# Kernel optimization log

Measured on AMD Instinct MI355X. Metric: run time of the kernel, lower is better.

The kernel has to match this reference:

```python
import jax, jax.numpy as jnp
import numpy as np

V, L, H, D, T, B = 32000, 8, 16, 1024, 1024, 2
HD = D // H
SCALE = 1.0 / float(np.sqrt(HD))


def setup_inputs() -> dict:
    key = jax.random.key(0)
    ks = jax.random.split(key, 8)
    s = 0.02
    def n(k, shape):
        return jax.random.normal(k, shape, jnp.float32) * s
    return {
        "input_ids": jax.random.randint(ks[0], (B, T), 0, V),
        "tok_emb": n(ks[1], (V, D)),            # tied with lm_head
        "pos_emb": n(ks[2], (T, D)),
        "ln1_w": jnp.ones((L, D)), "ln1_b": jnp.zeros((L, D)),
        "qkv_w": n(ks[3], (L, D, 3 * D)),       # no bias in qkv_proj
        "out_w": n(ks[4], (L, D, D)), "out_b": jnp.zeros((L, D)),
        "ln2_w": jnp.ones((L, D)), "ln2_b": jnp.zeros((L, D)),
        "fc1_w": n(ks[5], (L, D, 4 * D)), "fc1_b": jnp.zeros((L, 4 * D)),
        "fc2_w": n(ks[6], (L, 4 * D, D)), "fc2_b": jnp.zeros((L, D)),
        "lnf_w": jnp.ones((D,)), "lnf_b": jnp.zeros((D,)),
    }


def _ln(x, w, b):
    m = x.mean(-1, keepdims=True)
    v = x.var(-1, keepdims=True)
    return (x - m) * jax.lax.rsqrt(v + 1e-5) * w + b


def _gpt(input_ids, tok_emb, pos_emb, ln1_w, ln1_b, qkv_w, out_w, out_b,
         ln2_w, ln2_b, fc1_w, fc1_b, fc2_w, fc2_b, lnf_w, lnf_b):
    Bq, Tq = input_ids.shape
    x = tok_emb[input_ids] + pos_emb[:Tq][None]          # [B,T,D]
    causal = jnp.tril(jnp.ones((Tq, Tq), bool))          # [T,T]

    def layer(x, p):
        l1w, l1b, qw, ow, ob, l2w, l2b, f1w, f1b, f2w, f2b = p
        h = _ln(x, l1w, l1b)
        qkv = h @ qw                                     # [B,T,3D]
        q, k, v = jnp.split(qkv, 3, axis=-1)
        q = q.reshape(Bq, Tq, H, HD)
        k = k.reshape(Bq, Tq, H, HD)
        v = v.reshape(Bq, Tq, H, HD)
        att = jnp.einsum('bqhd,bkhd->bhqk', q, k) * SCALE
        att = jnp.where(causal, att, -jnp.inf)
        att = jax.nn.softmax(att, axis=-1)
        o = jnp.einsum('bhqk,bkhd->bqhd', att, v).reshape(Bq, Tq, D)
        x = x + o @ ow + ob
        h2 = _ln(x, l2w, l2b)
        x = x + jax.nn.gelu(h2 @ f1w + f1b, approximate=False) @ f2w + f2b
        return x, None

    x, _ = jax.lax.scan(layer, x, (ln1_w, ln1_b, qkv_w, out_w, out_b,
                                   ln2_w, ln2_b, fc1_w, fc1_b, fc2_w, fc2_b))
    x = _ln(x, lnf_w, lnf_b)
    return x @ tok_emb.T                                 # tied lm_head


def reference(input_ids, tok_emb, pos_emb, ln1_w, ln1_b, qkv_w, out_w, out_b,
              ln2_w, ln2_b, fc1_w, fc1_b, fc2_w, fc2_b, lnf_w, lnf_b):
    return _gpt(input_ids, tok_emb, pos_emb, ln1_w, ln1_b, qkv_w, out_w, out_b,
                ln2_w, ln2_b, fc1_w, fc1_b, fc2_w, fc2_b, lnf_w, lnf_b)
```

## Files before the change

### kernel.cpp

```cpp
#include <hip/hip_runtime.h>
#include <hip/hip_bf16.h>
#include <math.h>


#define DEV_INLINE __device__ __forceinline__

typedef float  f32x4  __attribute__((ext_vector_type(4)));
typedef __bf16 bf16x8 __attribute__((ext_vector_type(8)));
typedef short  s16x4  __attribute__((ext_vector_type(4)));
typedef short  s16x8  __attribute__((ext_vector_type(8)));
typedef unsigned int u32x4 __attribute__((ext_vector_type(4)));

#define BBATCH 2
#define TSEQ   1024
#define DMODEL 1024
#define NHEAD  16
#define HDIM   64
#define NLAYER 8
#define NVOCAB 32000
#define MTOK   (BBATCH*TSEQ)

DEV_INLINE short f2bf(float f) {
    __bf16 h = (__bf16)f;
    union { __bf16 h; short s; } u; u.h = h; return u.s;
}

typedef const __attribute__((address_space(1))) unsigned int* gas_t;
typedef __attribute__((address_space(3))) unsigned int* las_t;
DEV_INLINE void llds16(const void* g, void* l) {
    __builtin_amdgcn_global_load_lds((gas_t)g, (las_t)l, 16, 0, 0);
}

#define BAR()  asm volatile("s_barrier" ::: "memory")
#define VMW4() asm volatile("s_waitcnt vmcnt(4)" ::: "memory")
#define VMW2() asm volatile("s_waitcnt vmcnt(2)" ::: "memory")
#define VMW0() asm volatile("s_waitcnt vmcnt(0)" ::: "memory")

__global__ __launch_bounds__(256) void flash_k(
    const short* __restrict__ qkv, const short* __restrict__ Vt,
    short* __restrict__ O)
{
    const int qb = blockIdx.x;
    const int z  = blockIdx.y;
    const int zb = z >> 4, zh = z & 15;

    __shared__ short Qs[128 * 64];
    __shared__ short KP[128 * 136];
    __shared__ short Vs[64 * 128];

    const int tid  = threadIdx.x;
    const int w    = tid >> 6, lane = tid & 63;
    const int lr   = lane & 15, kg = lane >> 4;

    const long long qbase = (long long)zb * TSEQ * 3072;
    const short* Qg = qkv + qbase + zh * HDIM;
    const short* Kg = qkv + qbase + DMODEL + zh * HDIM;
    const short* Vg = Vt + (long long)z * (HDIM * TSEQ);

    const int sr   = tid >> 3, pc = tid & 7;
    const int lc   = pc ^ (sr & 7);
    const int sr16 = tid >> 4, pc16 = tid & 15;

    {
        const short* qp = Qg + (long long)(qb * 128 + sr) * 3072 + lc * 8;
        const short* kp = Kg + (long long)(0 + sr) * 3072 + lc * 8;
        #pragma unroll
        for (int it = 0; it < 4; ++it) {
            llds16(qp + (long long)it * 32 * 3072, Qs + tid * 8 + it * 2048);
            llds16(kp + (long long)it * 32 * 3072, KP + tid * 8 + it * 2048);
        }
        #pragma unroll
        for (int it = 0; it < 4; ++it) {
            const int r = it * 16 + sr16;
            const int lc2 = pc16 ^ (r & 7);
            llds16(Vg + (long long)r * TSEQ + 0 + lc2 * 8, Vs + tid * 8 + it * 2048);
        }
    }
    __syncthreads();
    bf16x8 afq[2][2];
    #pragma unroll
    for (int s = 0; s < 2; ++s)
        #pragma unroll
        for (int i = 0; i < 2; ++i) {
            const int r = w * 32 + i * 16 + lr;
            afq[s][i] = *(const bf16x8*)&Qs[r * 64 + (((s * 4 + kg) ^ (r & 7)) << 3)];
        }

    f32x4 aco[2][4] = {};
    float m_[2][4], l_[2][4];
    #pragma unroll
    for (int i = 0; i < 2; ++i)
        #pragma unroll
        for (int p = 0; p < 4; ++p) { m_[i][p] = -1e30f; l_[i][p] = 0.f; }

    const int nt = qb + 1;
    for (int t = 0; t < nt; ++t) {
        u32x4 kpre[4], vpre[4];
        const bool nx = (t + 1 < nt);
        if (nx) {
            const int kn = (t + 1) * 128;
            #pragma unroll
            for (int it = 0; it < 4; ++it)
                kpre[it] = *(const u32x4*)(Kg + (long long)(kn + sr + it * 32) * 3072 + lc * 8);
            #pragma unroll
            for (int it = 0; it < 4; ++it) {
                const int r = it * 16 + sr16;
                const int lc2 = pc16 ^ (r & 7);
                vpre[it] = *(const u32x4*)(Vg + (long long)r * TSEQ + kn + lc2 * 8);
            }
            __builtin_amdgcn_sched_barrier(0);
        }

        f32x4 acs[2][8] = {};
        #pragma unroll
        for (int s = 0; s < 2; ++s)
            #pragma unroll
            for (int j = 0; j < 8; ++j) {
                const int rk = j * 16 + lr;
                bf16x8 bk = *(const bf16x8*)&KP[rk * 64 + (((s * 4 + kg) ^ (rk & 7)) << 3)];
                #pragma unroll
                for (int i = 0; i < 2; ++i)
                    acs[i][j] = __builtin_amdgcn_mfma_f32_16x16x32_bf16(
                        afq[s][i], bk, acs[i][j], 0, 0, 0);
            }

        #pragma unroll
        for (int i = 0; i < 2; ++i)
            #pragma unroll
            for (int j = 0; j < 8; ++j)
                #pragma unroll
                for (int p = 0; p < 4; ++p) {
                    float v = acs[i][j][p] * 0.125f;
                    if (t == qb && (j * 16 + lr) > (w * 32 + i * 16 + kg * 4 + p))
                        v = -1e30f;
                    acs[i][j][p] = v;
                }

        float sc[2][4];
        #pragma unroll
        for (int i = 0; i < 2; ++i)
            #pragma unroll
            for (int p = 0; p < 4; ++p) {
                float r = acs[i][0][p];
                #pragma unroll
                for (int j = 1; j < 8; ++j) r = fmaxf(r, acs[i][j][p]);
                r = fmaxf(r, __shfl_xor(r, 1, 64));
                r = fmaxf(r, __shfl_xor(r, 2, 64));
                r = fmaxf(r, __shfl_xor(r, 4, 64));
                r = fmaxf(r, __shfl_xor(r, 8, 64));
                const float mn = fmaxf(m_[i][p], r);
                sc[i][p] = __expf(m_[i][p] - mn);
                m_[i][p] = mn;
            }
        #pragma unroll
        for (int i = 0; i < 2; ++i)
            #pragma unroll
            for (int j = 0; j < 8; ++j)
                #pragma unroll
                for (int p = 0; p < 4; ++p)
                    acs[i][j][p] = __expf(acs[i][j][p] - m_[i][p]);
        #pragma unroll
        for (int i = 0; i < 2; ++i)
            #pragma unroll
            for (int p = 0; p < 4; ++p) {
                float s = 0.f;
                #pragma unroll
                for (int j = 0; j < 8; ++j) s += acs[i][j][p];
                s += __shfl_xor(s, 1, 64);
                s += __shfl_xor(s, 2, 64);
                s += __shfl_xor(s, 4, 64);
                s += __shfl_xor(s, 8, 64);
                l_[i][p] = l_[i][p] * sc[i][p] + s;
            }
        #pragma unroll
        for (int i = 0; i < 2; ++i)
            #pragma unroll
            for (int j2 = 0; j2 < 4; ++j2)
                #pragma unroll
                for (int p = 0; p < 4; ++p)
                    aco[i][j2][p] *= sc[i][p];

        __syncthreads();

        #pragma unroll
        for (int i = 0; i < 2; ++i)
            #pragma unroll
            for (int j = 0; j < 8; ++j)
                #pragma unroll
                for (int p = 0; p < 4; ++p)
                    KP[(w * 32 + i * 16 + kg * 4 + p) * 136 + j * 16 + lr] =
                        f2bf(acs[i][j][p]);
        __syncthreads();

        #pragma unroll
        for (int ks = 0; ks < 4; ++ks) {
            bf16x8 pa[2], pb[4];
            #pragma unroll
            for (int i = 0; i < 2; ++i)
                pa[i] = *(const bf16x8*)&KP[(w * 32 + i * 16 + lr) * 136 + ks * 32 + kg * 8];
            #pragma unroll
            for (int j2 = 0; j2 < 4; ++j2) {
                const int d = j2 * 16 + lr;
                pb[j2] = *(const bf16x8*)&Vs[d * 128 + (((ks * 4 + kg) ^ (d & 7)) << 3)];
            }
            #pragma unroll
            for (int i = 0; i < 2; ++i)
                #pragma unroll
                for (int j2 = 0; j2 < 4; ++j2)
                    aco[i][j2] = __builtin_amdgcn_mfma_f32_16x16x32_bf16(
                        pa[i], pb[j2], aco[i][j2], 0, 0, 0);
        }
        __syncthreads();

        if (nx) {
            #pragma unroll
            for (int it = 0; it < 4; ++it)
                *(u32x4*)(KP + tid * 8 + it * 2048) = kpre[it];
            #pragma unroll
            for (int it = 0; it < 4; ++it)
                *(u32x4*)(Vs + tid * 8 + it * 2048) = vpre[it];
            __syncthreads();
        }
    }

    #pragma unroll
    for (int i = 0; i < 2; ++i)
        #pragma unroll
        for (int j2 = 0; j2 < 4; ++j2)
            #pragma unroll
            for (int p = 0; p < 4; ++p) {
                const int row = zb * TSEQ + qb * 128 + w * 32 + i * 16 + kg * 4 + p;
                const int col = zh * HDIM + j2 * 16 + lr;
                O[(long long)row * DMODEL + col] = f2bf(aco[i][j2][p] / l_[i][p]);
            }
}

__global__ __launch_bounds__(512, 2) void gemm256_k(
    const short* __restrict__ A, const short* __restrict__ B,
    float* __restrict__ C, int K, int lda, int ldb, int ldc, int gx)
{
    extern __shared__ short smem[];

    const int nwg = gridDim.x;
    int wg = blockIdx.x;
    int sw = (wg & 7) * (nwg >> 3) + (wg >> 3);
    const int bx = sw >> 3, by = sw & 7;
    const int bn0 = bx * 256, bm0 = by * 256;

    const int tid  = threadIdx.x;
    const int w    = tid >> 6, lane = tid & 63;
    const int wm   = w >> 2, wn = w & 3;
    const int lr   = lane & 15, kg = lane >> 4;

    const int r0  = tid >> 3;
    const int pc  = tid & 7;
    const int lc0 = pc ^ (r0 & 7);
    const int r1  = r0 + 64;
    const int lc1 = pc ^ (r1 & 7);

    f32x4 acc[2][2][4][2] = {};
    const int nk = K >> 6;

    auto stage = [&](int buf, int isA, int h, int kk) {
        const short* gp = isA ? A : B;
        const int    ld = isA ? lda : ldb;
        const long long rb = (long long)((isA ? bm0 : bn0) + h * 128);
        short* lp = smem + buf * 32768 + (isA ? 0 : 16384) + h * 8192;
        llds16(gp + (rb + r0) * ld + kk + lc0 * 8, lp + w * 512);
        llds16(gp + (rb + r1) * ld + kk + lc1 * 8, lp + 4096 + w * 512);
    };

#define PHASE(BUF, QM, QN, ISA, H, DOWAIT)                                      \
    do {                                                                        \
        const short* Ah = smem + (BUF) * 32768 + (QM) * 8192;                   \
        const short* Bh = smem + (BUF) * 32768 + 16384 + (QN) * 8192;           \
        bf16x8 af[2][4], bfr[2][2];                                             \
        _Pragma("unroll")                                                       \
        for (int s2 = 0; s2 < 2; ++s2) {                                        \
            _Pragma("unroll")                                                   \
            for (int i = 0; i < 4; ++i) {                                       \
                const int ra = wm * 64 + i * 16 + lr;                           \
                af[s2][i] = *(const bf16x8*)                                    \
                    &Ah[ra * 64 + (((s2 * 4 + kg) ^ (ra & 7)) << 3)];           \
            }                                                                   \
            _Pragma("unroll")                                                   \
            for (int j = 0; j < 2; ++j) {                                       \
                const int rb2 = wn * 32 + j * 16 + lr;                          \
                bfr[s2][j] = *(const bf16x8*)                                   \
                    &Bh[rb2 * 64 + (((s2 * 4 + kg) ^ (rb2 & 7)) << 3)];         \
            }                                                                   \
        }                                                                       \
        if (pf) stage(nb, ISA, H, kk);                                          \
        BAR();                                                                  \
        __builtin_amdgcn_s_setprio(1);                                          \
        _Pragma("unroll")                                                       \
        for (int s2 = 0; s2 < 2; ++s2)                                          \
            _Pragma("unroll")                                                   \
            for (int i = 0; i < 4; ++i)                                         \
                _Pragma("unroll")                                               \
                for (int j = 0; j < 2; ++j)                                     \
                    acc[QM][QN][i][j] = __builtin_amdgcn_mfma_f32_16x16x32_bf16(\
                        af[s2][i], bfr[s2][j], acc[QM][QN][i][j], 0, 0, 0);     \
        __builtin_amdgcn_s_setprio(0);                                          \
        DOWAIT;                                                                 \
        BAR();                                                                  \
    } while (0)

    stage(0, 1, 0, 0);
    stage(0, 0, 0, 0);
    stage(0, 1, 1, 0);
    stage(0, 0, 1, 0);
    if (nk > 1) { VMW4(); } else { VMW0(); }
    BAR();

    for (int t = 0; t < nk - 1; ++t) {
        const int  buf = t & 1, nb = buf ^ 1;
        const int  kk  = (t + 1) << 6;
        const bool pf  = true;
        PHASE(buf, 0, 0, 1, 0, VMW4());
        PHASE(buf, 1, 0, 0, 0, VMW4());
        PHASE(buf, 1, 1, 1, 1, (void)0);
        PHASE(buf, 0, 1, 0, 1, VMW4());
    }
    {
        const int  buf = (nk - 1) & 1, nb = buf ^ 1; (void)nb;
        const int  kk  = 0;
        const bool pf  = false;
        PHASE(buf, 0, 0, 1, 0, VMW2());
        PHASE(buf, 1, 0, 0, 0, VMW0());
        PHASE(buf, 1, 1, 1, 1, (void)0);
        PHASE(buf, 0, 1, 0, 1, (void)0);
    }
#undef PHASE

    #pragma unroll
    for (int qm = 0; qm < 2; ++qm)
        #pragma unroll
        for (int qn = 0; qn < 2; ++qn)
            #pragma unroll
            for (int i = 0; i < 4; ++i)
                #pragma unroll
                for (int j = 0; j < 2; ++j) {
                    const int gr = bm0 + qm * 128 + wm * 64 + i * 16 + kg * 4;
                    const int gc = bn0 + qn * 128 + wn * 32 + j * 16 + lr;
                    #pragma unroll
                    for (int p = 0; p < 4; ++p)
                        C[(long long)(gr + p) * ldc + gc] = acc[qm][qn][i][j][p];
                }
}

template<int BN, int EPI>
__global__ __launch_bounds__(256) void gemm_k(
    const short* __restrict__ Ag, const short* __restrict__ Bg,
    void* __restrict__ Cg, const float* __restrict__ bias,
    const float* __restrict__ resid,
    int M, int N, int K, int lda, int ldb, int ldc,
    long long sAz, long long sBz, long long sCz,
    float scale, int swz)
{
    int bx = blockIdx.x, by = blockIdx.y;
    if (swz) {
        const int gx = gridDim.x;
        const int nwg = gx * gridDim.y;
        if ((nwg & 7) == 0) {
            int wg = by * gx + bx;
            int wg2 = (wg & 7) * (nwg >> 3) + (wg >> 3);
            bx = wg2 % gx; by = wg2 / gx;
        }
    }
    const int bn0 = bx * BN, bm0 = by * 128;
    const int zz = blockIdx.z;

    const short* A = Ag + zz * sAz;
    const short* B = Bg + zz * sBz;

    __shared__ short Als[128 * 64];
    __shared__ short Bls[BN * 64];

    const int tid  = threadIdx.x;
    const int lane = tid & 63;
    const int wave = tid >> 6;
    constexpr int WMS = (BN == 128) ? 64 : 32;
    constexpr int MI  = (BN == 128) ? 4 : 2;
    constexpr int NJ  = 4;
    const int wm = (BN == 128) ? (wave >> 1) : wave;
    const int wn = (BN == 128) ? (wave & 1) : 0;
    const int lr = lane & 15, kg = lane >> 4;
    const int xv = (lr & 7) << 4;

    const int sr = tid >> 3;
    const int sc = (tid & 7) ^ (sr & 7);
    const short* aP = A + (long long)(bm0 + sr) * lda + sc * 8;
    const short* bP = B + (long long)(bn0 + sr) * ldb + sc * 8;
    short* aL = &Als[wave * 512];
    short* bL = &Bls[wave * 512];

    f32x4 acc[MI][NJ] = {};
    const int nk = K >> 6;

    for (int kt = 0; kt < nk; ++kt) {
        const int k0 = kt << 6;
        #pragma unroll
        for (int it = 0; it < 4; ++it)
            llds16(aP + (long long)it * 32 * lda + k0, aL + it * 2048);
        #pragma unroll
        for (int it = 0; it < BN / 32; ++it)
            llds16(bP + (long long)it * 32 * ldb + k0, bL + it * 2048);
        __syncthreads();

        #pragma unroll
        for (int s = 0; s < 2; ++s) {
            const int ofs = (((s << 6) | (kg << 4)) ^ xv) >> 1;
            bf16x8 af[MI], bf[NJ];
            #pragma unroll
            for (int i = 0; i < MI; ++i)
                af[i] = *(const bf16x8*)&Als[(wm * WMS + i * 16 + lr) * 64 + ofs];
            #pragma unroll
            for (int j = 0; j < NJ; ++j)
                bf[j] = *(const bf16x8*)&Bls[(wn * 64 + j * 16 + lr) * 64 + ofs];
            #pragma unroll
            for (int i = 0; i < MI; ++i)
                #pragma unroll
                for (int j = 0; j < NJ; ++j)
                    acc[i][j] = __builtin_amdgcn_mfma_f32_16x16x32_bf16(
                        af[i], bf[j], acc[i][j], 0, 0, 0);
        }
        __syncthreads();
    }

    short* Cs = (short*)Cg + zz * sCz;
    float* Cf = (float*)Cg + zz * sCz;
    #pragma unroll
    for (int i = 0; i < MI; ++i) {
        #pragma unroll
        for (int j = 0; j < NJ; ++j) {
            const int gr = bm0 + wm * WMS + i * 16 + kg * 4;
            const int gc = bn0 + wn * 64 + j * 16 + lr;
            #pragma unroll
            for (int p = 0; p < 4; ++p) {
                const long long off = (long long)(gr + p) * ldc + gc;
                float v = acc[i][j][p];
                if (EPI == 0) {
                    Cf[off] = v;
                } else if (EPI == 1) {
                    Cs[off] = f2bf(v * scale);
                } else if (EPI == 2) {
                    Cf[off] = v + bias[gc] + resid[off];
                } else {
                    v += bias[gc];
                    v = 0.5f * v * (1.0f + erff(v * 0.70710678118654752f));
                    Cs[off] = f2bf(v);
                }
            }
        }
    }
}

__global__ __launch_bounds__(256) void freduce_k(
    const float* __restrict__ p0, const float* __restrict__ p1,
    const float* __restrict__ bias, float* __restrict__ x)
{
    const long long idx = ((long long)blockIdx.x * 256 + threadIdx.x) * 4;
    const int col = (int)(idx & (DMODEL - 1));
    float4 a = *(const float4*)&p0[idx];
    float4 b = *(const float4*)&p1[idx];
    float4 c = *(const float4*)&x[idx];
    float4 bb = *(const float4*)&bias[col];
    float4 o;
    o.x = c.x + a.x + b.x + bb.x;
    o.y = c.y + a.y + b.y + bb.y;
    o.z = c.z + a.z + b.z + bb.z;
    o.w = c.w + a.w + b.w + bb.w;
    *(float4*)&x[idx] = o;
}

__global__ __launch_bounds__(256) void embed_k(
    const int* __restrict__ ids, const float* __restrict__ tok,
    const float* __restrict__ pos, float* __restrict__ x)
{
    const int gid = blockIdx.x * 256 + threadIdx.x;
    const int row = gid >> 8;
    const int c   = (gid & 255) << 2;
    const int t   = row & (TSEQ - 1);
    const int id  = ids[row];
    const float4 a = *(const float4*)&tok[(long long)id * DMODEL + c];
    const float4 p = *(const float4*)&pos[(long long)t * DMODEL + c];
    float4 o; o.x = a.x + p.x; o.y = a.y + p.y; o.z = a.z + p.z; o.w = a.w + p.w;
    *(float4*)&x[(long long)row * DMODEL + c] = o;
}

__global__ __launch_bounds__(256) void ln_k(
    const float* __restrict__ x, const float* __restrict__ w,
    const float* __restrict__ b, short* __restrict__ o)
{
    const int row  = blockIdx.x * 4 + (threadIdx.x >> 6);
    const int lane = threadIdx.x & 63;
    const float* xp = x + (long long)row * DMODEL + lane * 16;
    float4 v[4];
    #pragma unroll
    for (int q = 0; q < 4; ++q) v[q] = *(const float4*)(xp + q * 4);
    float s = 0.f, s2 = 0.f;
    #pragma unroll
    for (int q = 0; q < 4; ++q) {
        s  += v[q].x + v[q].y + v[q].z + v[q].w;
        s2 += v[q].x * v[q].x + v[q].y * v[q].y + v[q].z * v[q].z + v[q].w * v[q].w;
    }
    #pragma unroll
    for (int d = 1; d < 64; d <<= 1) {
        s  += __shfl_xor(s, d, 64);
        s2 += __shfl_xor(s2, d, 64);
    }
    const float mean = s * (1.0f / DMODEL);
    const float var  = s2 * (1.0f / DMODEL) - mean * mean;
    const float rs   = rsqrtf(var + 1e-5f);
    const float* wp = w + lane * 16;
    const float* bp = b + lane * 16;
    short ov[16];
    #pragma unroll
    for (int q = 0; q < 4; ++q) {
        float4 wv = *(const float4*)(wp + q * 4);
        float4 bv = *(const float4*)(bp + q * 4);
        ov[q * 4 + 0] = f2bf((v[q].x - mean) * rs * wv.x + bv.x);
        ov[q * 4 + 1] = f2bf((v[q].y - mean) * rs * wv.y + bv.y);
        ov[q * 4 + 2] = f2bf((v[q].z - mean) * rs * wv.z + bv.z);
        ov[q * 4 + 3] = f2bf((v[q].w - mean) * rs * wv.w + bv.w);
    }
    short* op = o + (long long)row * DMODEL + lane * 16;
    *(s16x8*)op       = *(s16x8*)&ov[0];
    *(s16x8*)(op + 8) = *(s16x8*)&ov[8];
}

template<typename T>
DEV_INLINE void tcvt_body(const T* sp, short* dp, int lds_, int ldd,
                          int bx, int by, short (*ls)[68], int t)
{
    const int tr0 = by * 64, tc0 = bx * 64;
    const int rr = t >> 4, cc = (t & 15) * 4;
    #pragma unroll
    for (int q = 0; q < 4; ++q) {
        const int r = q * 16 + rr;
        if constexpr (sizeof(T) == 4) {
            float4 v = *(const float4*)&sp[(long long)(tr0 + r) * lds_ + tc0 + cc];
            ls[cc + 0][r] = f2bf(v.x); ls[cc + 1][r] = f2bf(v.y);
            ls[cc + 2][r] = f2bf(v.z); ls[cc + 3][r] = f2bf(v.w);
        } else {
            s16x4 v = *(const s16x4*)&sp[(long long)(tr0 + r) * lds_ + tc0 + cc];
            ls[cc + 0][r] = v[0]; ls[cc + 1][r] = v[1];
            ls[cc + 2][r] = v[2]; ls[cc + 3][r] = v[3];
        }
    }
    __syncthreads();
    #pragma unroll
    for (int q = 0; q < 4; ++q) {
        const int c = q * 16 + rr;
        s16x4 v;
        v[0] = ls[c][cc]; v[1] = ls[c][cc + 1]; v[2] = ls[c][cc + 2]; v[3] = ls[c][cc + 3];
        *(s16x4*)&dp[(long long)(tc0 + c) * ldd + tr0 + cc] = v;
    }
}

template<typename T>
__global__ __launch_bounds__(256) void tcvt_k(
    const T* __restrict__ src, short* __restrict__ dst,
    int lds_, int ldd, int Hdiv,
    long long sSb, long long sSh, long long sDb, long long sDh)
{
    __shared__ short ls[64][68];
    const int z = blockIdx.z, zb = z / Hdiv, zh = z - zb * Hdiv;
    tcvt_body<T>(src + zb * sSb + zh * sSh, dst + zb * sDb + zh * sDh,
                 lds_, ldd, blockIdx.x, blockIdx.y, ls, threadIdx.x);
}

__global__ __launch_bounds__(256) void wcvt_k(
    const float* __restrict__ qw, const float* __restrict__ ow,
    const float* __restrict__ f1, const float* __restrict__ f2,
    short* __restrict__ wq, short* __restrict__ wo,
    short* __restrict__ w1, short* __restrict__ w2)
{
    __shared__ short ls[64][68];
    const int id = blockIdx.x;
    const float* src; short* dst; int lds_, ldd, bx, by;
    if (id < 768)       { src = qw; dst = wq; lds_ = 3072; ldd = 1024; bx = id % 48;  by = id / 48; }
    else if (id < 1024) { int i = id - 768;  src = ow; dst = wo; lds_ = 1024; ldd = 1024; bx = i % 16; by = i / 16; }
    else if (id < 2048) { int i = id - 1024; src = f1; dst = w1; lds_ = 4096; ldd = 1024; bx = i % 64; by = i / 64; }
    else                { int i = id - 2048; src = f2; dst = w2; lds_ = 1024; ldd = 4096; bx = i % 16; by = i / 16; }
    tcvt_body<float>(src, dst, lds_, ldd, bx, by, ls, threadIdx.x);
}

__global__ __launch_bounds__(256) void cvt_k(
    const float* __restrict__ s, short* __restrict__ d, int n4)
{
    int i = blockIdx.x * 256 + threadIdx.x;
    const int stride = gridDim.x * 256;
    for (; i < n4; i += stride) {
        float4 v = *(const float4*)&s[(long long)i * 4];
        s16x4 o = { f2bf(v.x), f2bf(v.y), f2bf(v.z), f2bf(v.w) };
        *(s16x4*)&d[(long long)i * 4] = o;
    }
}

extern "C" void kernel_launch(void* const* d_in, const int* in_sizes, int n_in,
                              void* d_out, int out_size, void* d_ws, size_t ws_size,
                              hipStream_t stream)
{
    const int*   ids  = (const int*)  d_in[0];
    const float* tok  = (const float*)d_in[1];
    const float* pos  = (const float*)d_in[2];
    const float* ln1w = (const float*)d_in[3];
    const float* ln1b = (const float*)d_in[4];
    const float* qkvw = (const float*)d_in[5];
    const float* outw = (const float*)d_in[6];
    const float* outb = (const float*)d_in[7];
    const float* ln2w = (const float*)d_in[8];
    const float* ln2b = (const float*)d_in[9];
    const float* fc1w = (const float*)d_in[10];
    const float* fc1b = (const float*)d_in[11];
    const float* fc2w = (const float*)d_in[12];
    const float* fc2b = (const float*)d_in[13];
    const float* lnfw = (const float*)d_in[14];
    const float* lnfb = (const float*)d_in[15];
    float* out = (float*)d_out;

    char* ws = (char*)d_ws;
    const size_t MB = 1024 * 1024;
    float* x    = (float*)(ws);
    short* hb   = (short*)(ws + 8  * MB);
    short* qkvb = (short*)(ws + 12 * MB);
    short* g    = (short*)(ws + 24 * MB);
    short* Vt   = (short*)(ws + 40 * MB);
    float* fp   = (float*)(ws + 44 * MB);
    short* tokb = (short*)(ws + 12 * MB);

    const bool big = ws_size >= (size_t)267 * MB;
    short* wq = (short*)(ws + 75 * MB);
    short *wo, *w1, *w2;
    if (big) {
        wo = (short*)(ws + 123 * MB);
        w1 = (short*)(ws + 139 * MB);
        w2 = (short*)(ws + 203 * MB);
    } else {
        wo = (short*)(ws + 81 * MB);
        w1 = (short*)(ws + 83 * MB);
        w2 = (short*)(ws + 91 * MB);
    }

    const long long LWQ = 3072LL * 1024, LWO = 1024LL * 1024;
    const long long LW1 = 4096LL * 1024, LW2 = 1024LL * 4096;

    hipFuncSetAttribute((const void*)gemm256_k,
                        hipFuncAttributeMaxDynamicSharedMemorySize, 131072);

    dim3 blk(256);
    embed_k<<<MTOK, blk, 0, stream>>>(ids, tok, pos, x);

    if (big) {
        tcvt_k<float><<<dim3(48, 16, 8), blk, 0, stream>>>(qkvw, wq, 3072, 1024, 1, LWQ, 0, LWQ, 0);
        tcvt_k<float><<<dim3(16, 16, 8), blk, 0, stream>>>(outw, wo, 1024, 1024, 1, LWO, 0, LWO, 0);
        tcvt_k<float><<<dim3(64, 16, 8), blk, 0, stream>>>(fc1w, w1, 4096, 1024, 1, LW1, 0, LW1, 0);
        tcvt_k<float><<<dim3(16, 64, 8), blk, 0, stream>>>(fc2w, w2, 1024, 4096, 1, LW2, 0, LW2, 0);
    }

    for (int l = 0; l < NLAYER; ++l) {
        short* wql = wq + (big ? l * LWQ : 0);
        short* wol = wo + (big ? l * LWO : 0);
        short* w1l = w1 + (big ? l * LW1 : 0);
        short* w2l = w2 + (big ? l * LW2 : 0);
        if (!big)
            wcvt_k<<<3072, blk, 0, stream>>>(
                qkvw + l * LWQ, outw + l * LWO, fc1w + l * LW1, fc2w + l * LW2,
                wql, wol, w1l, w2l);

        ln_k<<<MTOK / 4, blk, 0, stream>>>(x, ln1w + l * DMODEL, ln1b + l * DMODEL, hb);

        gemm_k<128, 1><<<dim3(24, 16, 1), blk, 0, stream>>>(
            hb, wql, qkvb, nullptr, nullptr,
            MTOK, 3 * DMODEL, DMODEL, DMODEL, DMODEL, 3 * DMODEL,
            0, 0, 0, 1.0f, 1);

        tcvt_k<short><<<dim3(1, 16, BBATCH * NHEAD), blk, 0, stream>>>(
            qkvb + 2 * DMODEL, Vt, 3 * DMODEL, TSEQ, NHEAD,
            (long long)TSEQ * 3 * DMODEL, HDIM,
            (long long)NHEAD * HDIM * TSEQ, (long long)HDIM * TSEQ);

        flash_k<<<dim3(8, BBATCH * NHEAD), blk, 0, stream>>>(qkvb, Vt, hb);

        gemm_k<64, 2><<<dim3(16, 16, 1), blk, 0, stream>>>(
            hb, wol, x, outb + l * DMODEL, x,
            MTOK, DMODEL, DMODEL, DMODEL, DMODEL, DMODEL,
            0, 0, 0, 1.0f, 1);

        ln_k<<<MTOK / 4, blk, 0, stream>>>(x, ln2w + l * DMODEL, ln2b + l * DMODEL, hb);

        gemm_k<128, 3><<<dim3(32, 16, 1), blk, 0, stream>>>(
            hb, w1l, g, fc1b + (long long)l * 4 * DMODEL, nullptr,
            MTOK, 4 * DMODEL, DMODEL, DMODEL, DMODEL, 4 * DMODEL,
            0, 0, 0, 1.0f, 1);

        gemm_k<128, 0><<<dim3(8, 16, 2), blk, 0, stream>>>(
            g, w2l, fp, nullptr, nullptr,
            MTOK, DMODEL, 2048, 4 * DMODEL, 4 * DMODEL, DMODEL,
            2048, 2048, (long long)MTOK * DMODEL, 1.0f, 1);
        freduce_k<<<MTOK, blk, 0, stream>>>(
            fp, fp + (long long)MTOK * DMODEL, fc2b + l * DMODEL, x);
    }

    ln_k<<<MTOK / 4, blk, 0, stream>>>(x, lnfw, lnfb, hb);

    cvt_k<<<2048, blk, 0, stream>>>(tok, tokb, NVOCAB * DMODEL / 4);

    gemm256_k<<<dim3((NVOCAB / 256) * (MTOK / 256)), dim3(512), 131072, stream>>>(
        hb, tokb, out, DMODEL, DMODEL, DMODEL, NVOCAB, NVOCAB / 256);
}
```

Before: 1.786 ms.

## Double-buffer GEMM LDS staging and fuse residual reduce with LayerNorm

The generic GEMM now double-buffers its LDS tiles, issuing the next K-tile's global-to-LDS loads before computing the current one and dropping one barrier per iteration. The out-projection switches to a split-K GEMM with two partial outputs. Those partials are combined in a new kernel that adds bias and residual and also applies the following LayerNorm, so the standalone LN kernels and the embed kernel are merged away. This cuts launches and extra passes over the activations, at the cost of doubled LDS use (which may lower occupancy) and an extra fp32 partial buffer write and read for the out-projection.

```diff
diff --git a/kernel.cpp b/kernel.cpp
--- a/kernel.cpp
+++ b/kernel.cpp
@@ -35,6 +35,17 @@
 #define VMW4() asm volatile("s_waitcnt vmcnt(4)" ::: "memory")
 #define VMW2() asm volatile("s_waitcnt vmcnt(2)" ::: "memory")
 #define VMW0() asm volatile("s_waitcnt vmcnt(0)" ::: "memory")
+
+DEV_INLINE float block_sum(float v) {
+    __shared__ float sb[4];
+    #pragma unroll
+    for (int o = 32; o > 0; o >>= 1) v += __shfl_down(v, o, 64);
+    if ((threadIdx.x & 63) == 0) sb[threadIdx.x >> 6] = v;
+    __syncthreads();
+    float r = sb[0] + sb[1] + sb[2] + sb[3];
+    __syncthreads();
+    return r;
+}
 
 __global__ __launch_bounds__(256) void flash_k(
     const short* __restrict__ qkv, const short* __restrict__ Vt,
@@ -353,7 +364,6 @@
 __global__ __launch_bounds__(256) void gemm_k(
     const short* __restrict__ Ag, const short* __restrict__ Bg,
     void* __restrict__ Cg, const float* __restrict__ bias,
-    const float* __restrict__ resid,
     int M, int N, int K, int lda, int ldb, int ldc,
     long long sAz, long long sBz, long long sCz,
     float scale, int swz)
@@ -374,8 +384,8 @@
     const short* A = Ag + zz * sAz;
     const short* B = Bg + zz * sBz;
 
-    __shared__ short Als[128 * 64];
-    __shared__ short Bls[BN * 64];
+    __shared__ short Als[2][128 * 64];
+    __shared__ short Bls[2][BN * 64];
 
     const int tid  = threadIdx.x;
     const int lane = tid & 63;
@@ -392,21 +402,28 @@
     const int sc = (tid & 7) ^ (sr & 7);
     const short* aP = A + (long long)(bm0 + sr) * lda + sc * 8;
     const short* bP = B + (long long)(bn0 + sr) * ldb + sc * 8;
-    short* aL = &Als[wave * 512];
-    short* bL = &Bls[wave * 512];
 
     f32x4 acc[MI][NJ] = {};
     const int nk = K >> 6;
 
-    for (int kt = 0; kt < nk; ++kt) {
+    auto stage = [&](int buf, int kt) {
         const int k0 = kt << 6;
+        short* aL = &Als[buf][wave * 512];
+        short* bL = &Bls[buf][wave * 512];
         #pragma unroll
         for (int it = 0; it < 4; ++it)
             llds16(aP + (long long)it * 32 * lda + k0, aL + it * 2048);
         #pragma unroll
         for (int it = 0; it < BN / 32; ++it)
             llds16(bP + (long long)it * 32 * ldb + k0, bL + it * 2048);
-        __syncthreads();
+    };
+
+    stage(0, 0);
+    __syncthreads();
+
+    for (int kt = 0; kt < nk; ++kt) {
+        const int cb = kt & 1;
+        if (kt + 1 < nk) stage(cb ^ 1, kt + 1);
 
         #pragma unroll
         for (int s = 0; s < 2; ++s) {
@@ -414,10 +431,10 @@
             bf16x8 af[MI], bf[NJ];
             #pragma unroll
             for (int i = 0; i < MI; ++i)
-                af[i] = *(const bf16x8*)&Als[(wm * WMS + i * 16 + lr) * 64 + ofs];
+                af[i] = *(const bf16x8*)&Als[cb][(wm * WMS + i * 16 + lr) * 64 + ofs];
             #pragma unroll
             for (int j = 0; j < NJ; ++j)
-                bf[j] = *(const bf16x8*)&Bls[(wn * 64 + j * 16 + lr) * 64 + ofs];
+                bf[j] = *(const bf16x8*)&Bls[cb][(wn * 64 + j * 16 + lr) * 64 + ofs];
             #pragma unroll
             for (int i = 0; i < MI; ++i)
                 #pragma unroll
@@ -444,8 +461,6 @@
                     Cf[off] = v;
                 } else if (EPI == 1) {
                     Cs[off] = f2bf(v * scale);
-                } else if (EPI == 2) {
-                    Cf[off] = v + bias[gc] + resid[off];
                 } else {
                     v += bias[gc];
                     v = 0.5f * v * (1.0f + erff(v * 0.70710678118654752f));
@@ -456,78 +471,73 @@
     }
 }
 
-__global__ __launch_bounds__(256) void freduce_k(
+__global__ __launch_bounds__(256) void fredln_k(
     const float* __restrict__ p0, const float* __restrict__ p1,
-    const float* __restrict__ bias, float* __restrict__ x)
-{
-    const long long idx = ((long long)blockIdx.x * 256 + threadIdx.x) * 4;
-    const int col = (int)(idx & (DMODEL - 1));
-    float4 a = *(const float4*)&p0[idx];
-    float4 b = *(const float4*)&p1[idx];
-    float4 c = *(const float4*)&x[idx];
-    float4 bb = *(const float4*)&bias[col];
-    float4 o;
-    o.x = c.x + a.x + b.x + bb.x;
-    o.y = c.y + a.y + b.y + bb.y;
-    o.z = c.z + a.z + b.z + bb.z;
-    o.w = c.w + a.w + b.w + bb.w;
-    *(float4*)&x[idx] = o;
-}
-
-__global__ __launch_bounds__(256) void embed_k(
-    const int* __restrict__ ids, const float* __restrict__ tok,
-    const float* __restrict__ pos, float* __restrict__ x)
-{
-    const int gid = blockIdx.x * 256 + threadIdx.x;
-    const int row = gid >> 8;
-    const int c   = (gid & 255) << 2;
-    const int t   = row & (TSEQ - 1);
-    const int id  = ids[row];
-    const float4 a = *(const float4*)&tok[(long long)id * DMODEL + c];
-    const float4 p = *(const float4*)&pos[(long long)t * DMODEL + c];
-    float4 o; o.x = a.x + p.x; o.y = a.y + p.y; o.z = a.z + p.z; o.w = a.w + p.w;
-    *(float4*)&x[(long long)row * DMODEL + c] = o;
-}
-
-__global__ __launch_bounds__(256) void ln_k(
-    const float* __restrict__ x, const float* __restrict__ w,
-    const float* __restrict__ b, short* __restrict__ o)
-{
-    const int row  = blockIdx.x * 4 + (threadIdx.x >> 6);
-    const int lane = threadIdx.x & 63;
-    const float* xp = x + (long long)row * DMODEL + lane * 16;
-    float4 v[4];
-    #pragma unroll
-    for (int q = 0; q < 4; ++q) v[q] = *(const float4*)(xp + q * 4);
-    float s = 0.f, s2 = 0.f;
-    #pragma unroll
-    for (int q = 0; q < 4; ++q) {
-        s  += v[q].x + v[q].y + v[q].z + v[q].w;
-        s2 += v[q].x * v[q].x + v[q].y * v[q].y + v[q].z * v[q].z + v[q].w * v[q].w;
-    }
-    #pragma unroll
-    for (int d = 1; d < 64; d <<= 1) {
-        s  += __shfl_xor(s, d, 64);
-        s2 += __shfl_xor(s2, d, 64);
-    }
+    const float* __restrict__ bias, float* __restrict__ x,
+    const float* __restrict__ lw, const float* __restrict__ lb,
+    short* __restrict__ o)
+{
+    const int row = blockIdx.x;
+    const long long base = (long long)row * DMODEL;
+    const int i = threadIdx.x * 4;
+    float4 a  = *(const float4*)&p0[base + i];
+    float4 b  = *(const float4*)&p1[base + i];
+    float4 c  = *(const float4*)&x[base + i];
+    float4 bb = *(const float4*)&bias[i];
+    float4 v;
+    v.x = c.x + a.x + b.x + bb.x;
+    v.y = c.y + a.y + b.y + bb.y;
+    v.z = c.z + a.z + b.z + bb.z;
+    v.w = c.w + a.w + b.w + bb.w;
+    *(float4*)&x[base + i] = v;
+    float s  = v.x + v.y + v.z + v.w;
+    float s2 = v.x * v.x + v.y * v.y + v.z * v.z + v.w * v.w;
+    s  = block_sum(s);
+    s2 = block_sum(s2);
     const float mean = s * (1.0f / DMODEL);
     const float var  = s2 * (1.0f / DMODEL) - mean * mean;
     const float rs   = rsqrtf(var + 1e-5f);
-    const float* wp = w + lane * 16;
-    const float* bp = b + lane * 16;
-    short ov[16];
-    #pragma unroll
-    for (int q = 0; q < 4; ++q) {
-        float4 wv = *(const float4*)(wp + q * 4);
-        float4 bv = *(const float4*)(bp + q * 4);
-        ov[q * 4 + 0] = f2bf((v[q].x - mean) * rs * wv.x + bv.x);
-        ov[q * 4 + 1] = f2bf((v[q].y - mean) * rs * wv.y + bv.y);
-        ov[q * 4 + 2] = f2bf((v[q].z - mean) * rs * wv.z + bv.z);
-        ov[q * 4 + 3] = f2bf((v[q].w - mean) * rs * wv.w + bv.w);
-    }
-    short* op = o + (long long)row * DMODEL + lane * 16;
-    *(s16x8*)op       = *(s16x8*)&ov[0];
-    *(s16x8*)(op + 8) = *(s16x8*)&ov[8];
+    float4 wv = *(const float4*)&lw[i];
+    float4 bv = *(const float4*)&lb[i];
+    s16x4 ov;
+    ov[0] = f2bf((v.x - mean) * rs * wv.x + bv.x);
+    ov[1] = f2bf((v.y - mean) * rs * wv.y + bv.y);
+    ov[2] = f2bf((v.z - mean) * rs * wv.z + bv.z);
+    ov[3] = f2bf((v.w - mean) * rs * wv.w + bv.w);
+    *(s16x4*)&o[base + i] = ov;
+}
+
+__global__ __launch_bounds__(256) void embedln_k(
+    const int* __restrict__ ids, const float* __restrict__ tok,
+    const float* __restrict__ pos, float* __restrict__ x,
+    const float* __restrict__ lw, const float* __restrict__ lb,
+    short* __restrict__ o)
+{
+    const int row = blockIdx.x;
+    const int t   = row & (TSEQ - 1);
+    const int id  = ids[row];
+    const int i   = threadIdx.x * 4;
+    const long long base = (long long)row * DMODEL;
+    float4 a = *(const float4*)&tok[(long long)id * DMODEL + i];
+    float4 p = *(const float4*)&pos[(long long)t * DMODEL + i];
+    float4 v;
+    v.x = a.x + p.x; v.y = a.y + p.y; v.z = a.z + p.z; v.w = a.w + p.w;
+    *(float4*)&x[base + i] = v;
+    float s  = v.x + v.y + v.z + v.w;
+    float s2 = v.x * v.x + v.y * v.y + v.z * v.z + v.w * v.w;
+    s  = block_sum(s);
+    s2 = block_sum(s2);
+    const float mean = s * (1.0f / DMODEL);
+    const float var  = s2 * (1.0f / DMODEL) - mean * mean;
+    const float rs   = rsqrtf(var + 1e-5f);
+    float4 wv = *(const float4*)&lw[i];
+    float4 bv = *(const float4*)&lb[i];
+    s16x4 ov;
+    ov[0] = f2bf((v.x - mean) * rs * wv.x + bv.x);
+    ov[1] = f2bf((v.y - mean) * rs * wv.y + bv.y);
+    ov[2] = f2bf((v.z - mean) * rs * wv.z + bv.z);
+    ov[3] = f2bf((v.w - mean) * rs * wv.w + bv.w);
+    *(s16x4*)&o[base + i] = ov;
 }
 
 template<typename T>
@@ -646,12 +656,13 @@
 
     const long long LWQ = 3072LL * 1024, LWO = 1024LL * 1024;
     const long long LW1 = 4096LL * 1024, LW2 = 1024LL * 4096;
+    const long long MD  = (long long)MTOK * DMODEL;
 
     hipFuncSetAttribute((const void*)gemm256_k,
                         hipFuncAttributeMaxDynamicSharedMemorySize, 131072);
 
     dim3 blk(256);
-    embed_k<<<MTOK, blk, 0, stream>>>(ids, tok, pos, x);
+    embedln_k<<<MTOK, blk, 0, stream>>>(ids, tok, pos, x, ln1w, ln1b, hb);
 
     if (big) {
         tcvt_k<float><<<dim3(48, 16, 8), blk, 0, stream>>>(qkvw, wq, 3072, 1024, 1, LWQ, 0, LWQ, 0);
@@ -670,10 +681,8 @@
                 qkvw + l * LWQ, outw + l * LWO, fc1w + l * LW1, fc2w + l * LW2,
                 wql, wol, w1l, w2l);
 
-        ln_k<<<MTOK / 4, blk, 0, stream>>>(x, ln1w + l * DMODEL, ln1b + l * DMODEL, hb);
-
         gemm_k<128, 1><<<dim3(24, 16, 1), blk, 0, stream>>>(
-            hb, wql, qkvb, nullptr, nullptr,
+            hb, wql, qkvb, nullptr,
             MTOK, 3 * DMODEL, DMODEL, DMODEL, DMODEL, 3 * DMODEL,
             0, 0, 0, 1.0f, 1);
 
@@ -684,27 +693,28 @@
 
         flash_k<<<dim3(8, BBATCH * NHEAD), blk, 0, stream>>>(qkvb, Vt, hb);
 
-        gemm_k<64, 2><<<dim3(16, 16, 1), blk, 0, stream>>>(
-            hb, wol, x, outb + l * DMODEL, x,
-            MTOK, DMODEL, DMODEL, DMODEL, DMODEL, DMODEL,
-            0, 0, 0, 1.0f, 1);
-
-        ln_k<<<MTOK / 4, blk, 0, stream>>>(x, ln2w + l * DMODEL, ln2b + l * DMODEL, hb);
+        gemm_k<128, 0><<<dim3(8, 16, 2), blk, 0, stream>>>(
+            hb, wol, fp, nullptr,
+            MTOK, DMODEL, 512, DMODEL, DMODEL, DMODEL,
+            512, 512, MD, 1.0f, 1);
+        fredln_k<<<MTOK, blk, 0, stream>>>(
+            fp, fp + MD, outb + l * DMODEL, x,
+            ln2w + l * DMODEL, ln2b + l * DMODEL, hb);
 
         gemm_k<128, 3><<<dim3(32, 16, 1), blk, 0, stream>>>(
-            hb, w1l, g, fc1b + (long long)l * 4 * DMODEL, nullptr,
+            hb, w1l, g, fc1b + (long long)l * 4 * DMODEL,
             MTOK, 4 * DMODEL, DMODEL, DMODEL, DMODEL, 4 * DMODEL,
             0, 0, 0, 1.0f, 1);
 
         gemm_k<128, 0><<<dim3(8, 16, 2), blk, 0, stream>>>(
-            g, w2l, fp, nullptr, nullptr,
+            g, w2l, fp, nullptr,
             MTOK, DMODEL, 2048, 4 * DMODEL, 4 * DMODEL, DMODEL,
-            2048, 2048, (long long)MTOK * DMODEL, 1.0f, 1);
-        freduce_k<<<MTOK, blk, 0, stream>>>(
-            fp, fp + (long long)MTOK * DMODEL, fc2b + l * DMODEL, x);
-    }
-
-    ln_k<<<MTOK / 4, blk, 0, stream>>>(x, lnfw, lnfb, hb);
+            2048, 2048, MD, 1.0f, 1);
+        const float* nlw = (l < 7) ? ln1w + (l + 1) * DMODEL : lnfw;
+        const float* nlb = (l < 7) ? ln1b + (l + 1) * DMODEL : lnfb;
+        fredln_k<<<MTOK, blk, 0, stream>>>(
+            fp, fp + MD, fc2b + l * DMODEL, x, nlw, nlb, hb);
+    }
 
     cvt_k<<<2048, blk, 0, stream>>>(tok, tokb, NVOCAB * DMODEL / 4);
 
```

Result: faster. 1.675 ms (-6.2%).
